# Optimization experiments

Measured on AMD Instinct MI355X. Metric: run time of the kernel, lower is better.

## Reference

```python
import jax, jax.numpy as jnp
import numpy as np

NUM_BANDS = 30
SPLIT_FREQ = 30
M_PARAM = 1
DIM = 2048
BATCH = 16384


def _dct_mat(N):
    # Orthonormal DCT-II matrix D: dct(x) = x @ D.T, idct(y) = y @ D
    n = np.arange(N, dtype=np.float64)
    kk = n[:, None]
    M = np.cos(np.pi * (n + 0.5) * kk / N)
    s = np.full(N, np.sqrt(2.0 / N))
    s[0] = np.sqrt(1.0 / N)
    return jnp.asarray((M * s[:, None]).astype(np.float32))


def _band_scale(freq_weights, k, N):
    # Precompute the per-frequency scale vector the torch loop applies band-by-band.
    pts = np.linspace(0, N - 1, NUM_BANDS + 1).astype(np.int64)  # torch .long() truncation
    scale = jnp.ones((N,), dtype=freq_weights.dtype)
    for i in range(NUM_BANDS):
        s, e = int(pts[i]), int(pts[i + 1])
        if e <= SPLIT_FREQ:
            f = 1.0 + freq_weights[i] * k * (1.0 - i / NUM_BANDS)
        else:
            f = 1.0 - freq_weights[i] * k * (1.0 - (i - NUM_BANDS // M_PARAM) / NUM_BANDS)
        scale = scale.at[s:e].set(f)  # bands are disjoint; base is 1
    return scale


def setup_inputs() -> dict:
    key = jax.random.key(0)
    ks = jax.random.split(key, 6)
    g = 0.02  # small init like xavier_uniform with gain 0.5
    return {
        "x": jax.random.normal(ks[0], (BATCH, DIM), dtype=jnp.float32),
        "freq_weights": jnp.ones((NUM_BANDS,), dtype=jnp.float32),
        "k": jnp.float32(0.3),
        "W1": jax.random.normal(ks[1], (1024, DIM), dtype=jnp.float32) * g,
        "b1": jnp.zeros((1024,), dtype=jnp.float32),
        "W2": jax.random.normal(ks[2], (512, 1024), dtype=jnp.float32) * g,
        "b2": jnp.zeros((512,), dtype=jnp.float32),
        "Wmu": jax.random.normal(ks[3], (256, 512), dtype=jnp.float32) * g,
        "bmu": jnp.zeros((256,), dtype=jnp.float32),
        "Wlv": jax.random.normal(ks[4], (256, 512), dtype=jnp.float32) * g,
        "blv": jnp.zeros((256,), dtype=jnp.float32),
    }


def reference(x, freq_weights, k, W1, b1, W2, b2, Wmu, bmu, Wlv, blv):
    N = x.shape[-1]
    D = _dct_mat(N)
    # DCT -> per-band reweight -> IDCT, fused as two matmuls and one vector multiply
    xd = (x @ D.T) * _band_scale(freq_weights, k, N)
    xe = xd @ D
    h = jax.nn.relu(xe @ W1.T + b1)
    h = jax.nn.relu(h @ W2.T + b2)
    mu = h @ Wmu.T + bmu
    logvar = h @ Wlv.T + blv
    return (mu, logvar)
```

## Files before the change

### kernel.cpp

```cpp
#include <hip/hip_runtime.h>
#include <hip/hip_bf16.h>
#include <math.h>

#define DIM 2048
#define BATCH 16384

typedef __attribute__((ext_vector_type(8))) short short8;
typedef __attribute__((ext_vector_type(4))) float floatx4;
typedef unsigned short ushort_t;
typedef unsigned int uint_t;

__device__ __forceinline__ ushort_t f2bf(float f) {
    union { float f; unsigned u; } v; v.f = f;
    unsigned r = v.u + 0x7FFFu + ((v.u >> 16) & 1u);
    return (ushort_t)(r >> 16);
}

__device__ __forceinline__ uint_t cvt2bf(float a, float b) {
    __hip_bfloat162 h = __float22bfloat162_rn(float2{a, b});
    union { __hip_bfloat162 h; uint_t u; } v; v.h = h;
    return v.u;
}

__global__ void k_scale(const float* __restrict__ fw, const float* __restrict__ kp,
                        float* __restrict__ s) {
    int n = blockIdx.x * blockDim.x + threadIdx.x;
    if (n >= DIM) return;
    float kv = kp[0];
    float f = 1.0f;
    for (int i = 0; i < 30; ++i) {
        long s0 = (long)((double)i       * (double)(DIM - 1) / 30.0);
        long e0 = (long)((double)(i + 1) * (double)(DIM - 1) / 30.0);
        if (n >= s0 && n < e0) {
            if (e0 <= 30)
                f = 1.0f + fw[i] * kv * (1.0f - (float)i / 30.0f);
            else
                f = 1.0f - fw[i] * kv * (1.0f - (float)(i - 30) / 30.0f);
        }
    }
    s[n] = f;
}

__global__ void k_gen_d(ushort_t* __restrict__ D, ushort_t* __restrict__ Dt) {
    int idx = blockIdx.x * blockDim.x + threadIdx.x;
    int r = idx >> 11;
    int c = idx & (DIM - 1);
    const float w  = 7.6699039394282058e-4f;
    const float s0 = 0.02209708691207961f;
    const float s1 = 0.03125f;
    int m1 = ((2 * c + 1) * r) & (4 * DIM - 1);
    int m2 = ((2 * r + 1) * c) & (4 * DIM - 1);
    float v1 = cosf(w * (float)m1) * (r == 0 ? s0 : s1);
    float v2 = cosf(w * (float)m2) * (c == 0 ? s0 : s1);
    D[idx]  = f2bf(v1);
    Dt[idx] = f2bf(v2);
}

#define U_W1   262144
#define U_W2    65536
#define U_WH    16384
__global__ void k_cast_w(const float* __restrict__ W1, const float* __restrict__ W2,
                         const float* __restrict__ Wmu, const float* __restrict__ Wlv,
                         ushort_t* __restrict__ W1bf, ushort_t* __restrict__ W2bf,
                         ushort_t* __restrict__ Wcat) {
    int i = blockIdx.x * blockDim.x + threadIdx.x;
    const float* src; ushort_t* dst; int u;
    if (i < U_W1)                    { src = W1;  dst = W1bf;             u = i; }
    else if (i < U_W1 + U_W2)        { src = W2;  dst = W2bf;             u = i - U_W1; }
    else if (i < U_W1 + U_W2 + U_WH) { src = Wmu; dst = Wcat;             u = i - U_W1 - U_W2; }
    else                             { src = Wlv; dst = Wcat + 8 * U_WH;  u = i - U_W1 - U_W2 - U_WH; }
    const float4* p = reinterpret_cast<const float4*>(src) + 2 * (size_t)u;
    float4 a = p[0], b = p[1];
    short8 r;
    r[0] = (short)f2bf(a.x); r[1] = (short)f2bf(a.y);
    r[2] = (short)f2bf(a.z); r[3] = (short)f2bf(a.w);
    r[4] = (short)f2bf(b.x); r[5] = (short)f2bf(b.y);
    r[6] = (short)f2bf(b.z); r[7] = (short)f2bf(b.w);
    *reinterpret_cast<short8*>(dst + 8 * (size_t)u) = r;
}

template<int TM, int TN, int EPI, bool AF32>
__device__ __forceinline__ void gemm_core(
        const ushort_t* __restrict__ A, const float* __restrict__ Af,
        const ushort_t* __restrict__ B,
        ushort_t* __restrict__ Cb, float* __restrict__ Cf,
        const float* __restrict__ ep0, const float* __restrict__ ep1,
        int M, int N, int K) {
    constexpr int BM = 32 * TM;
    constexpr int BN = 32 * TN;
    __shared__ __align__(16) ushort_t As[BM * 32];
    __shared__ __align__(16) ushort_t Bs[BN * 32];

    const int tid  = threadIdx.x;
    const int lane = tid & 63;
    const int wave = tid >> 6;
    const int wm   = wave >> 1;
    const int wn   = wave & 1;
    const int q    = lane >> 4;
    const int l16  = lane & 15;

    const int tilesM = M / BM;
    const int tilesN = N / BN;
    const int bid = (int)blockIdx.x;
    const int xcd = bid & 7;
    const int j   = bid >> 3;
    const int bm  = xcd * (tilesM >> 3) + j / tilesN;
    const int bn  = j % tilesN;

    floatx4 acc[TM][TN];
    #pragma unroll
    for (int i = 0; i < TM; ++i)
        #pragma unroll
        for (int jj = 0; jj < TN; ++jj)
            acc[i][jj] = (floatx4){0.f, 0.f, 0.f, 0.f};

    const long aBase = (long)bm * BM * K;
    const long bBase = (long)bn * BN * K;

    float4 pf[4];
    const float* abase = nullptr;
    if constexpr (AF32) {
        abase = Af + aBase + (long)(tid >> 3) * K + (tid & 7) * 4;
        #pragma unroll
        for (int i = 0; i < 4; ++i)
            pf[i] = *reinterpret_cast<const float4*>(abase + (long)i * 32 * K);
    }

    for (int kt = 0; kt < K; kt += 32) {
        __syncthreads();
        if constexpr (AF32) {
            const int rowb = tid >> 3, fseg = tid & 7;
            #pragma unroll
            for (int i = 0; i < 4; ++i) {
                int row  = rowb + i * 32;
                int lseg = (fseg >> 1) ^ ((row >> 1) & 3);
                uint2 w;
                w.x = cvt2bf(pf[i].x, pf[i].y);
                w.y = cvt2bf(pf[i].z, pf[i].w);
                *reinterpret_cast<uint2*>(As + row * 32 + lseg * 8 + (fseg & 1) * 4) = w;
            }
        } else {
            #pragma unroll
            for (int i = 0; i < BM / 64; ++i) {
                int idx = tid + i * 256;
                int row = idx >> 2, seg = idx & 3;
                int gseg = seg ^ ((row >> 1) & 3);
                const ushort_t* g = A + aBase + (long)row * K + kt + gseg * 8;
                __builtin_amdgcn_global_load_lds(
                    (const __attribute__((address_space(1))) void*)g,
                    (__attribute__((address_space(3))) void*)(As + idx * 8),
                    16, 0, 0);
            }
        }
        #pragma unroll
        for (int i = 0; i < BN / 64; ++i) {
            int idx = tid + i * 256;
            int row = idx >> 2, seg = idx & 3;
            int gseg = seg ^ ((row >> 1) & 3);
            const ushort_t* g = B + bBase + (long)row * K + kt + gseg * 8;
            __builtin_amdgcn_global_load_lds(
                (const __attribute__((address_space(1))) void*)g,
                (__attribute__((address_space(3))) void*)(Bs + idx * 8),
                16, 0, 0);
        }
        __syncthreads();

        short8 af[TM], bfr[TN];
        #pragma unroll
        for (int t = 0; t < TM; ++t) {
            int srow = wm * TM * 16 + t * 16 + l16;
            int rseg = q ^ ((srow >> 1) & 3);
            af[t] = *reinterpret_cast<const short8*>(&As[srow * 32 + rseg * 8]);
        }
        #pragma unroll
        for (int t = 0; t < TN; ++t) {
            int srow = wn * TN * 16 + t * 16 + l16;
            int rseg = q ^ ((srow >> 1) & 3);
            bfr[t] = *reinterpret_cast<const short8*>(&Bs[srow * 32 + rseg * 8]);
        }
        if constexpr (AF32) {
            if (kt + 32 < K) {
                const float* ab = abase + kt + 32;
                #pragma unroll
                for (int i = 0; i < 4; ++i)
                    pf[i] = *reinterpret_cast<const float4*>(ab + (long)i * 32 * K);
            }
        }
        #pragma unroll
        for (int i = 0; i < TM; ++i)
            #pragma unroll
            for (int jj = 0; jj < TN; ++jj)
                acc[i][jj] = __builtin_amdgcn_mfma_f32_16x16x32_bf16(
                    af[i], bfr[jj], acc[i][jj], 0, 0, 0);
    }

    #pragma unroll
    for (int i = 0; i < TM; ++i) {
        #pragma unroll
        for (int jj = 0; jj < TN; ++jj) {
            #pragma unroll
            for (int r = 0; r < 4; ++r) {
                int row = bm * BM + wm * TM * 16 + i * 16 + q * 4 + r;
                int col = bn * BN + wn * TN * 16 + jj * 16 + l16;
                float v = acc[i][jj][r];
                if constexpr (EPI == 0) {
                    Cb[(long)row * N + col] = f2bf(v * ep0[col]);
                } else if constexpr (EPI == 1) {
                    Cb[(long)row * N + col] = f2bf(v);
                } else if constexpr (EPI == 2) {
                    v += ep0[col];
                    v = v > 0.f ? v : 0.f;
                    Cb[(long)row * N + col] = f2bf(v);
                } else {
                    const int half = N >> 1;
                    if (col < half)
                        Cf[(long)row * half + col] = v + ep0[col];
                    else
                        Cf[(long)M * half + (long)row * half + (col - half)] = v + ep1[col - half];
                }
            }
        }
    }
}

__global__ __launch_bounds__(256) void g0_w1d(const ushort_t* A, const ushort_t* B,
        ushort_t* Cb, const float* ep0, int M, int N, int K) {
    gemm_core<2, 2, 0, false>(A, nullptr, B, Cb, nullptr, ep0, nullptr, M, N, K);
}
__global__ __launch_bounds__(256) void g1_m1(const ushort_t* A, const ushort_t* B,
        ushort_t* Cb, int M, int N, int K) {
    gemm_core<2, 2, 1, false>(A, nullptr, B, Cb, nullptr, nullptr, nullptr, M, N, K);
}
__global__ __launch_bounds__(256) void g2_xm1(const float* Af, const ushort_t* B,
        ushort_t* Cb, const float* ep0, int M, int N, int K) {
    gemm_core<4, 4, 2, true>(nullptr, Af, B, Cb, nullptr, ep0, nullptr, M, N, K);
}
__global__ __launch_bounds__(256) void g3_h2(const ushort_t* A, const ushort_t* B,
        ushort_t* Cb, const float* ep0, int M, int N, int K) {
    gemm_core<4, 4, 2, false>(A, nullptr, B, Cb, nullptr, ep0, nullptr, M, N, K);
}
__global__ __launch_bounds__(256) void g4_head(const ushort_t* A, const ushort_t* B,
        float* Cf, const float* ep0, const float* ep1, int M, int N, int K) {
    gemm_core<4, 4, 3, false>(A, nullptr, B, nullptr, Cf, ep0, ep1, M, N, K);
}

extern "C" void kernel_launch(void* const* d_in, const int* in_sizes, int n_in,
                              void* d_out, int out_size, void* d_ws, size_t ws_size,
                              hipStream_t stream) {
    const float* x   = (const float*)d_in[0];
    const float* fw  = (const float*)d_in[1];
    const float* kp  = (const float*)d_in[2];
    const float* W1  = (const float*)d_in[3];
    const float* b1  = (const float*)d_in[4];
    const float* W2  = (const float*)d_in[5];
    const float* b2  = (const float*)d_in[6];
    const float* Wmu = (const float*)d_in[7];
    const float* bmu = (const float*)d_in[8];
    const float* Wlv = (const float*)d_in[9];
    const float* blv = (const float*)d_in[10];
    float* out = (float*)d_out;

    char* ws = (char*)d_ws;
    const size_t MB = 1024 * 1024;
    ushort_t* W1bf = (ushort_t*)(ws + 0);
    ushort_t* Dbf  = (ushort_t*)(ws + 4  * MB);
    ushort_t* Dtbf = (ushort_t*)(ws + 12 * MB);
    ushort_t* T1sT = (ushort_t*)(ws + 20 * MB);
    ushort_t* H1   = (ushort_t*)(ws + 0);
    ushort_t* H2   = (ushort_t*)(ws + 32 * MB);
    ushort_t* M1T  = (ushort_t*)(ws + 48 * MB);
    ushort_t* W2bf = (ushort_t*)(ws + 52 * MB);
    ushort_t* Wcat = (ushort_t*)(ws + 53 * MB);
    float*    svec = (float*)   (ws + 54 * MB);

    hipLaunchKernelGGL(k_scale, dim3(DIM / 256), dim3(256), 0, stream, fw, kp, svec);
    hipLaunchKernelGGL(k_gen_d, dim3(DIM * DIM / 256), dim3(256), 0, stream, Dbf, Dtbf);
    hipLaunchKernelGGL(k_cast_w, dim3((U_W1 + U_W2 + 2 * U_WH) / 256), dim3(256), 0, stream,
                       W1, W2, Wmu, Wlv, W1bf, W2bf, Wcat);

    hipLaunchKernelGGL(g0_w1d, dim3((1024 / 64) * (2048 / 64)), dim3(256), 0, stream,
                       W1bf, Dbf, T1sT, svec, 1024, 2048, 2048);
    hipLaunchKernelGGL(g1_m1, dim3((1024 / 64) * (2048 / 64)), dim3(256), 0, stream,
                       T1sT, Dtbf, M1T, 1024, 2048, 2048);
    hipLaunchKernelGGL(g2_xm1, dim3((BATCH / 128) * (1024 / 128)), dim3(256), 0, stream,
                       x, M1T, H1, b1, BATCH, 1024, 2048);
    hipLaunchKernelGGL(g3_h2, dim3((BATCH / 128) * (512 / 128)), dim3(256), 0, stream,
                       H1, W2bf, H2, b2, BATCH, 512, 1024);
    hipLaunchKernelGGL(g4_head, dim3((BATCH / 128) * (512 / 128)), dim3(256), 0, stream,
                       H2, Wcat, out, bmu, blv, BATCH, 512, 512);

    (void)in_sizes; (void)n_in; (void)out_size; (void)ws_size;
}
```

Baseline: 455.2 us.

## Split-K precompute GEMMs, pre-cast x to bf16, widen BK for main GEMM

The two DCT-folding GEMMs now use 128x128 tiles with a 4-way split-K that writes fp32 partials, and a separate reduction kernel sums them, applies the band scale and casts to bf16. The input x is cast to bf16 in its own pass, so the big GEMM can stream A through global_load_lds with BK=64 instead of converting fp32 in registers. D generation uses the fast __cosf. This adds extra kernels and a full x read/write round trip, plus fp32 partial buffers, in exchange for better occupancy and a simpler main loop.

Result: faster. 406.2 us (-10.8%).

```diff
diff --git a/kernel.cpp b/kernel.cpp
--- a/kernel.cpp
+++ b/kernel.cpp
@@ -6,20 +6,14 @@
 #define BATCH 16384
 
 typedef __attribute__((ext_vector_type(8))) short short8;
+typedef __attribute__((ext_vector_type(4))) short short4v;
 typedef __attribute__((ext_vector_type(4))) float floatx4;
 typedef unsigned short ushort_t;
-typedef unsigned int uint_t;
 
 __device__ __forceinline__ ushort_t f2bf(float f) {
     union { float f; unsigned u; } v; v.f = f;
     unsigned r = v.u + 0x7FFFu + ((v.u >> 16) & 1u);
     return (ushort_t)(r >> 16);
-}
-
-__device__ __forceinline__ uint_t cvt2bf(float a, float b) {
-    __hip_bfloat162 h = __float22bfloat162_rn(float2{a, b});
-    union { __hip_bfloat162 h; uint_t u; } v; v.h = h;
-    return v.u;
 }
 
 __global__ void k_scale(const float* __restrict__ fw, const float* __restrict__ kp,
@@ -50,8 +44,8 @@
     const float s1 = 0.03125f;
     int m1 = ((2 * c + 1) * r) & (4 * DIM - 1);
     int m2 = ((2 * r + 1) * c) & (4 * DIM - 1);
-    float v1 = cosf(w * (float)m1) * (r == 0 ? s0 : s1);
-    float v2 = cosf(w * (float)m2) * (c == 0 ? s0 : s1);
+    float v1 = __cosf(w * (float)m1) * (r == 0 ? s0 : s1);
+    float v2 = __cosf(w * (float)m2) * (c == 0 ? s0 : s1);
     D[idx]  = f2bf(v1);
     Dt[idx] = f2bf(v2);
 }
@@ -79,17 +73,51 @@
     *reinterpret_cast<short8*>(dst + 8 * (size_t)u) = r;
 }
 
-template<int TM, int TN, int EPI, bool AF32>
+__global__ void k_cast_x(const float* __restrict__ in, ushort_t* __restrict__ out) {
+    int i = blockIdx.x * blockDim.x + threadIdx.x;
+    const float4* p = reinterpret_cast<const float4*>(in) + 2 * (size_t)i;
+    float4 a = p[0], b = p[1];
+    short8 r;
+    r[0] = (short)f2bf(a.x); r[1] = (short)f2bf(a.y);
+    r[2] = (short)f2bf(a.z); r[3] = (short)f2bf(a.w);
+    r[4] = (short)f2bf(b.x); r[5] = (short)f2bf(b.y);
+    r[6] = (short)f2bf(b.z); r[7] = (short)f2bf(b.w);
+    *reinterpret_cast<short8*>(out + 8 * (size_t)i) = r;
+}
+
+__global__ void k_red(const float* __restrict__ P, ushort_t* __restrict__ out,
+                      const float* __restrict__ scale, int n4, int n4row) {
+    int i = blockIdx.x * blockDim.x + threadIdx.x;
+    const float4* p = reinterpret_cast<const float4*>(P);
+    float4 a = p[i], b = p[i + n4], c = p[i + 2 * n4], d = p[i + 3 * n4];
+    float4 s;
+    s.x = a.x + b.x + c.x + d.x;
+    s.y = a.y + b.y + c.y + d.y;
+    s.z = a.z + b.z + c.z + d.z;
+    s.w = a.w + b.w + c.w + d.w;
+    if (scale) {
+        float4 sc = reinterpret_cast<const float4*>(scale)[i & (n4row - 1)];
+        s.x *= sc.x; s.y *= sc.y; s.z *= sc.z; s.w *= sc.w;
+    }
+    short4v o;
+    o[0] = (short)f2bf(s.x); o[1] = (short)f2bf(s.y);
+    o[2] = (short)f2bf(s.z); o[3] = (short)f2bf(s.w);
+    *reinterpret_cast<short4v*>(out + 4 * (size_t)i) = o;
+}
+
+template<int TM, int TN, int BK, int EPI, bool SK4>
 __device__ __forceinline__ void gemm_core(
-        const ushort_t* __restrict__ A, const float* __restrict__ Af,
-        const ushort_t* __restrict__ B,
+        const ushort_t* __restrict__ A, const ushort_t* __restrict__ B,
         ushort_t* __restrict__ Cb, float* __restrict__ Cf,
         const float* __restrict__ ep0, const float* __restrict__ ep1,
-        int M, int N, int K) {
+        int M, int N, int K, int KC) {
     constexpr int BM = 32 * TM;
     constexpr int BN = 32 * TN;
-    __shared__ __align__(16) ushort_t As[BM * 32];
-    __shared__ __align__(16) ushort_t Bs[BN * 32];
+    constexpr int SEGS = BK / 8;
+    constexpr int RSH  = (BK == 32) ? 1 : 0;
+    constexpr int SSH  = (SEGS == 4) ? 2 : 3;
+    __shared__ __align__(16) ushort_t As[BM * BK];
+    __shared__ __align__(16) ushort_t Bs[BN * BK];
 
     const int tid  = threadIdx.x;
     const int lane = tid & 63;
@@ -101,7 +129,9 @@
 
     const int tilesM = M / BM;
     const int tilesN = N / BN;
-    const int bid = (int)blockIdx.x;
+    int bid = (int)blockIdx.x;
+    int sk = 0;
+    if constexpr (SK4) { int nt = tilesM * tilesN; sk = bid / nt; bid = bid % nt; }
     const int xcd = bid & 7;
     const int j   = bid >> 3;
     const int bm  = xcd * (tilesM >> 3) + j / tilesN;
@@ -114,49 +144,28 @@
         for (int jj = 0; jj < TN; ++jj)
             acc[i][jj] = (floatx4){0.f, 0.f, 0.f, 0.f};
 
-    const long aBase = (long)bm * BM * K;
-    const long bBase = (long)bn * BN * K;
-
-    float4 pf[4];
-    const float* abase = nullptr;
-    if constexpr (AF32) {
-        abase = Af + aBase + (long)(tid >> 3) * K + (tid & 7) * 4;
-        #pragma unroll
-        for (int i = 0; i < 4; ++i)
-            pf[i] = *reinterpret_cast<const float4*>(abase + (long)i * 32 * K);
-    }
-
-    for (int kt = 0; kt < K; kt += 32) {
+    const long aBase = (long)bm * BM * K + (long)sk * KC;
+    const long bBase = (long)bn * BN * K + (long)sk * KC;
+    const int  KLOOP = SK4 ? KC : K;
+
+    for (int kt = 0; kt < KLOOP; kt += BK) {
         __syncthreads();
-        if constexpr (AF32) {
-            const int rowb = tid >> 3, fseg = tid & 7;
-            #pragma unroll
-            for (int i = 0; i < 4; ++i) {
-                int row  = rowb + i * 32;
-                int lseg = (fseg >> 1) ^ ((row >> 1) & 3);
-                uint2 w;
-                w.x = cvt2bf(pf[i].x, pf[i].y);
-                w.y = cvt2bf(pf[i].z, pf[i].w);
-                *reinterpret_cast<uint2*>(As + row * 32 + lseg * 8 + (fseg & 1) * 4) = w;
-            }
-        } else {
-            #pragma unroll
-            for (int i = 0; i < BM / 64; ++i) {
-                int idx = tid + i * 256;
-                int row = idx >> 2, seg = idx & 3;
-                int gseg = seg ^ ((row >> 1) & 3);
-                const ushort_t* g = A + aBase + (long)row * K + kt + gseg * 8;
-                __builtin_amdgcn_global_load_lds(
-                    (const __attribute__((address_space(1))) void*)g,
-                    (__attribute__((address_space(3))) void*)(As + idx * 8),
-                    16, 0, 0);
-            }
-        }
-        #pragma unroll
-        for (int i = 0; i < BN / 64; ++i) {
+        #pragma unroll
+        for (int i = 0; i < BM * BK / 2048; ++i) {
             int idx = tid + i * 256;
-            int row = idx >> 2, seg = idx & 3;
-            int gseg = seg ^ ((row >> 1) & 3);
+            int row = idx >> SSH, seg = idx & (SEGS - 1);
+            int gseg = seg ^ ((row >> RSH) & (SEGS - 1));
+            const ushort_t* g = A + aBase + (long)row * K + kt + gseg * 8;
+            __builtin_amdgcn_global_load_lds(
+                (const __attribute__((address_space(1))) void*)g,
+                (__attribute__((address_space(3))) void*)(As + idx * 8),
+                16, 0, 0);
+        }
+        #pragma unroll
+        for (int i = 0; i < BN * BK / 2048; ++i) {
+            int idx = tid + i * 256;
+            int row = idx >> SSH, seg = idx & (SEGS - 1);
+            int gseg = seg ^ ((row >> RSH) & (SEGS - 1));
             const ushort_t* g = B + bBase + (long)row * K + kt + gseg * 8;
             __builtin_amdgcn_global_load_lds(
                 (const __attribute__((address_space(1))) void*)g,
@@ -165,33 +174,28 @@
         }
         __syncthreads();
 
-        short8 af[TM], bfr[TN];
-        #pragma unroll
-        for (int t = 0; t < TM; ++t) {
-            int srow = wm * TM * 16 + t * 16 + l16;
-            int rseg = q ^ ((srow >> 1) & 3);
-            af[t] = *reinterpret_cast<const short8*>(&As[srow * 32 + rseg * 8]);
-        }
-        #pragma unroll
-        for (int t = 0; t < TN; ++t) {
-            int srow = wn * TN * 16 + t * 16 + l16;
-            int rseg = q ^ ((srow >> 1) & 3);
-            bfr[t] = *reinterpret_cast<const short8*>(&Bs[srow * 32 + rseg * 8]);
-        }
-        if constexpr (AF32) {
-            if (kt + 32 < K) {
-                const float* ab = abase + kt + 32;
+        #pragma unroll
+        for (int ks = 0; ks < BK / 32; ++ks) {
+            short8 af[TM], bfr[TN];
+            #pragma unroll
+            for (int t = 0; t < TM; ++t) {
+                int srow = wm * TM * 16 + t * 16 + l16;
+                int rseg = (ks * 4 + q) ^ ((srow >> RSH) & (SEGS - 1));
+                af[t] = *reinterpret_cast<const short8*>(&As[srow * BK + rseg * 8]);
+            }
+            #pragma unroll
+            for (int t = 0; t < TN; ++t) {
+                int srow = wn * TN * 16 + t * 16 + l16;
+                int rseg = (ks * 4 + q) ^ ((srow >> RSH) & (SEGS - 1));
+                bfr[t] = *reinterpret_cast<const short8*>(&Bs[srow * BK + rseg * 8]);
+            }
+            #pragma unroll
+            for (int i = 0; i < TM; ++i)
                 #pragma unroll
-                for (int i = 0; i < 4; ++i)
-                    pf[i] = *reinterpret_cast<const float4*>(ab + (long)i * 32 * K);
-            }
-        }
-        #pragma unroll
-        for (int i = 0; i < TM; ++i)
-            #pragma unroll
-            for (int jj = 0; jj < TN; ++jj)
-                acc[i][jj] = __builtin_amdgcn_mfma_f32_16x16x32_bf16(
-                    af[i], bfr[jj], acc[i][jj], 0, 0, 0);
+                for (int jj = 0; jj < TN; ++jj)
+                    acc[i][jj] = __builtin_amdgcn_mfma_f32_16x16x32_bf16(
+                        af[i], bfr[jj], acc[i][jj], 0, 0, 0);
+        }
     }
 
     #pragma unroll
@@ -211,37 +215,39 @@
                     v += ep0[col];
                     v = v > 0.f ? v : 0.f;
                     Cb[(long)row * N + col] = f2bf(v);
-                } else {
+                } else if constexpr (EPI == 3) {
                     const int half = N >> 1;
                     if (col < half)
                         Cf[(long)row * half + col] = v + ep0[col];
                     else
                         Cf[(long)M * half + (long)row * half + (col - half)] = v + ep1[col - half];
+                } else {
+                    Cf[(long)sk * M * N + (long)row * N + col] = v;
                 }
             }
         }
     }
 }
 
-__global__ __launch_bounds__(256) void g0_w1d(const ushort_t* A, const ushort_t* B,
+__global__ __launch_bounds__(256) void g0p_sk(const ushort_t* A, const ushort_t* B,
+        float* P, int M, int N, int K, int KC) {
+    gemm_core<4, 4, 32, 4, true>(A, B, nullptr, P, nullptr, nullptr, M, N, K, KC);
+}
+__global__ __launch_bounds__(256) void g1p_sk(const ushort_t* A, const ushort_t* B,
+        float* P, int M, int N, int K, int KC) {
+    gemm_core<4, 4, 32, 4, true>(A, B, nullptr, P, nullptr, nullptr, M, N, K, KC);
+}
+__global__ __launch_bounds__(256) void g2_xm1(const ushort_t* A, const ushort_t* B,
         ushort_t* Cb, const float* ep0, int M, int N, int K) {
-    gemm_core<2, 2, 0, false>(A, nullptr, B, Cb, nullptr, ep0, nullptr, M, N, K);
-}
-__global__ __launch_bounds__(256) void g1_m1(const ushort_t* A, const ushort_t* B,
-        ushort_t* Cb, int M, int N, int K) {
-    gemm_core<2, 2, 1, false>(A, nullptr, B, Cb, nullptr, nullptr, nullptr, M, N, K);
-}
-__global__ __launch_bounds__(256) void g2_xm1(const float* Af, const ushort_t* B,
-        ushort_t* Cb, const float* ep0, int M, int N, int K) {
-    gemm_core<4, 4, 2, true>(nullptr, Af, B, Cb, nullptr, ep0, nullptr, M, N, K);
+    gemm_core<4, 4, 64, 2, false>(A, B, Cb, nullptr, ep0, nullptr, M, N, K, 0);
 }
 __global__ __launch_bounds__(256) void g3_h2(const ushort_t* A, const ushort_t* B,
         ushort_t* Cb, const float* ep0, int M, int N, int K) {
-    gemm_core<4, 4, 2, false>(A, nullptr, B, Cb, nullptr, ep0, nullptr, M, N, K);
+    gemm_core<4, 4, 32, 2, false>(A, B, Cb, nullptr, ep0, nullptr, M, N, K, 0);
 }
 __global__ __launch_bounds__(256) void g4_head(const ushort_t* A, const ushort_t* B,
         float* Cf, const float* ep0, const float* ep1, int M, int N, int K) {
-    gemm_core<4, 4, 3, false>(A, nullptr, B, nullptr, Cf, ep0, ep1, M, N, K);
+    gemm_core<4, 4, 32, 3, false>(A, B, nullptr, Cf, ep0, ep1, M, N, K, 0);
 }
 
 extern "C" void kernel_launch(void* const* d_in, const int* in_sizes, int n_in,
@@ -263,27 +269,36 @@
     char* ws = (char*)d_ws;
     const size_t MB = 1024 * 1024;
     ushort_t* W1bf = (ushort_t*)(ws + 0);
-    ushort_t* Dbf  = (ushort_t*)(ws + 4  * MB);
-    ushort_t* Dtbf = (ushort_t*)(ws + 12 * MB);
-    ushort_t* T1sT = (ushort_t*)(ws + 20 * MB);
+    ushort_t* Dbf  = (ushort_t*)(ws + 4   * MB);
+    ushort_t* Dtbf = (ushort_t*)(ws + 12  * MB);
+    ushort_t* T1sT = (ushort_t*)(ws + 20  * MB);
     ushort_t* H1   = (ushort_t*)(ws + 0);
-    ushort_t* H2   = (ushort_t*)(ws + 32 * MB);
-    ushort_t* M1T  = (ushort_t*)(ws + 48 * MB);
-    ushort_t* W2bf = (ushort_t*)(ws + 52 * MB);
-    ushort_t* Wcat = (ushort_t*)(ws + 53 * MB);
-    float*    svec = (float*)   (ws + 54 * MB);
+    float*    P    = (float*)   (ws + 32  * MB);
+    ushort_t* Xbf  = (ushort_t*)(ws + 32  * MB);
+    ushort_t* H2   = (ushort_t*)(ws + 96  * MB);
+    ushort_t* M1T  = (ushort_t*)(ws + 112 * MB);
+    ushort_t* W2bf = (ushort_t*)(ws + 116 * MB);
+    ushort_t* Wcat = (ushort_t*)(ws + 117 * MB);
+    float*    svec = (float*)   (ws + 118 * MB);
 
     hipLaunchKernelGGL(k_scale, dim3(DIM / 256), dim3(256), 0, stream, fw, kp, svec);
     hipLaunchKernelGGL(k_gen_d, dim3(DIM * DIM / 256), dim3(256), 0, stream, Dbf, Dtbf);
     hipLaunchKernelGGL(k_cast_w, dim3((U_W1 + U_W2 + 2 * U_WH) / 256), dim3(256), 0, stream,
                        W1, W2, Wmu, Wlv, W1bf, W2bf, Wcat);
 
-    hipLaunchKernelGGL(g0_w1d, dim3((1024 / 64) * (2048 / 64)), dim3(256), 0, stream,
-                       W1bf, Dbf, T1sT, svec, 1024, 2048, 2048);
-    hipLaunchKernelGGL(g1_m1, dim3((1024 / 64) * (2048 / 64)), dim3(256), 0, stream,
-                       T1sT, Dtbf, M1T, 1024, 2048, 2048);
+    hipLaunchKernelGGL(g0p_sk, dim3(8 * 16 * 4), dim3(256), 0, stream,
+                       W1bf, Dbf, P, 1024, 2048, 2048, 512);
+    hipLaunchKernelGGL(k_red, dim3(1024 * 2048 / 4 / 256), dim3(256), 0, stream,
+                       P, T1sT, svec, 1024 * 2048 / 4, 2048 / 4);
+    hipLaunchKernelGGL(g1p_sk, dim3(8 * 16 * 4), dim3(256), 0, stream,
+                       T1sT, Dtbf, P, 1024, 2048, 2048, 512);
+    hipLaunchKernelGGL(k_red, dim3(1024 * 2048 / 4 / 256), dim3(256), 0, stream,
+                       P, M1T, nullptr, 1024 * 2048 / 4, 2048 / 4);
+
+    hipLaunchKernelGGL(k_cast_x, dim3(BATCH * DIM / 8 / 256), dim3(256), 0, stream, x, Xbf);
+
     hipLaunchKernelGGL(g2_xm1, dim3((BATCH / 128) * (1024 / 128)), dim3(256), 0, stream,
-                       x, M1T, H1, b1, BATCH, 1024, 2048);
+                       Xbf, M1T, H1, b1, BATCH, 1024, 2048);
     hipLaunchKernelGGL(g3_h2, dim3((BATCH / 128) * (512 / 128)), dim3(256), 0, stream,
                        H1, W2bf, H2, b2, BATCH, 512, 1024);
     hipLaunchKernelGGL(g4_head, dim3((BATCH / 128) * (512 / 128)), dim3(256), 0, stream,
```
